# Performance work log

Measured on AMD Instinct MI355X. Metric: run time of the kernel, lower is better.

The kernel has to match this reference:

```python
import jax, jax.numpy as jnp
import numpy as np

B, S, E, H = 8, 1024, 512, 8
NEG = -1e10


def setup_inputs() -> dict:
    key = jax.random.key(0)
    ks = jax.random.split(key, 8)
    k = jax.random.normal(ks[0], (B, S, E), dtype=jnp.float32)
    v = jax.random.normal(ks[1], (B, S, E), dtype=jnp.float32)
    q = jax.random.normal(ks[2], (B, S, E), dtype=jnp.float32)
    # causal mask, broadcastable like torch masked_fill
    mask = jnp.tril(jnp.ones((S, S), dtype=jnp.int32))[None, None]
    sc = 1.0 / np.sqrt(E)
    Wk = jax.random.normal(ks[3], (H * E, E), dtype=jnp.float32) * sc
    Wq = jax.random.normal(ks[4], (H * E, E), dtype=jnp.float32) * sc
    Wv = jax.random.normal(ks[5], (H * E, E), dtype=jnp.float32) * sc
    Wo = jax.random.normal(ks[6], (E, H * E), dtype=jnp.float32) * (1.0 / np.sqrt(H * E))
    bo = jnp.zeros((E,), dtype=jnp.float32)
    return {"k": k, "v": v, "q": q, "mask": mask,
            "Wk": Wk, "Wq": Wq, "Wv": Wv, "Wo": Wo, "bo": bo}


def reference(k, v, q, mask, Wk, Wq, Wv, Wo, bo):
    b, q_len, e = q.shape
    k_len, v_len = k.shape[1], v.shape[1]
    h = Wk.shape[0] // e
    scale = jnp.sqrt(jnp.asarray(e // h, dtype=jnp.float32))
    # projections E -> H*E (torch Linear: x @ W.T)
    wk = (k @ Wk.T).reshape(b, h, k_len, e)   # raw reshape, matches torch .view
    wq = (q @ Wq.T).reshape(b, h, q_len, e)
    wv = (v @ Wv.T).reshape(b, h, v_len, e)
    energy = jnp.einsum('bhqe,bhke->bhqk', wq, wk)
    energy = jnp.where(mask == 0, NEG, energy)  # mask applied BEFORE scaling, as in source
    energy = energy / scale
    attn = jax.nn.softmax(energy, axis=-1)
    f = jnp.einsum('bhqk,bhke->bhqe', attn, wv)
    f = jnp.transpose(f, (0, 2, 1, 3)).reshape(b, q_len, h * e)
    return f @ Wo.T + bo
```

## Files before the change

### kernel.cpp

```cpp
#include <hip/hip_runtime.h>


typedef _Float16 half8 __attribute__((ext_vector_type(8)));
typedef _Float16 half4v __attribute__((ext_vector_type(4)));
typedef float f32x4 __attribute__((ext_vector_type(4)));

typedef __attribute__((address_space(3))) unsigned int lds_u32_t;
typedef __attribute__((address_space(1))) unsigned int g_u32_t;

__device__ __forceinline__ void glds16(const void* g, void* l) {
  __builtin_amdgcn_global_load_lds((const g_u32_t*)g, (lds_u32_t*)l, 16, 0, 0);
}

template <int NT>
__device__ __forceinline__ void gemm128x256_core(const _Float16* __restrict__ A,
                                                 const _Float16* __restrict__ B,
                                                 int lda, int ldb,
                                                 _Float16* smem, f32x4 (&acc)[4][8]) {
  int tid = (int)threadIdx.x;
  int w = tid >> 6, lane = tid & 63;
  int wr2 = (w >> 1) * 32;
  int wc2 = (w & 1) * 64;
  int lr = lane & 15, hi = lane >> 4;
  int sp = ((((lane & 1) << 2) + hi) ^ ((lr >> 1) & 7)) << 3;
  int aBase = (wr2 + (lr >> 1)) * 64 + sp;
  int bBase = 4096 + (wc2 + (lr >> 1)) * 64 + sp;

  int srcA[2], srcB[4], dstA[2], dstB[4];
#pragma unroll
  for (int e = 0; e < 2; e++) {
    int X = e * 4096 + tid * 16;
    int rp = X >> 7;
    int s = ((X >> 4) & 7) ^ (rp & 7);
    srcA[e] = (2 * rp + (s >> 2)) * lda + ((s & 3) << 3);
    dstA[e] = e * 2048 + w * 512;
  }
#pragma unroll
  for (int e = 0; e < 4; e++) {
    int X = e * 4096 + tid * 16;
    int rp = X >> 7;
    int s = ((X >> 4) & 7) ^ (rp & 7);
    srcB[e] = (2 * rp + (s >> 2)) * ldb + ((s & 3) << 3);
    dstB[e] = 4096 + e * 2048 + w * 512;
  }

#pragma unroll
  for (int e = 0; e < 2; e++) glds16(A + srcA[e], smem + dstA[e]);
#pragma unroll
  for (int e = 0; e < 4; e++) glds16(B + srcB[e], smem + dstB[e]);
  if (NT > 1) {
#pragma unroll
    for (int e = 0; e < 2; e++) glds16(A + srcA[e] + 32, smem + 12288 + dstA[e]);
#pragma unroll
    for (int e = 0; e < 4; e++) glds16(B + srcB[e] + 32, smem + 12288 + dstB[e]);
  }

#pragma unroll
  for (int t = 0; t < NT; t++) {
    if (t + 1 < NT) asm volatile("s_waitcnt vmcnt(6)" ::: "memory");
    else            asm volatile("s_waitcnt vmcnt(0)" ::: "memory");
    __builtin_amdgcn_s_barrier();
    __builtin_amdgcn_sched_barrier(0);
    const _Float16* As = smem + (t % 3) * 12288;
    half8 a[4], b[4], c[4];
#pragma unroll
    for (int ni = 0; ni < 4; ni++) b[ni] = *(const half8*)&As[bBase + ni * 512];
#pragma unroll
    for (int mi = 0; mi < 4; mi++) a[mi] = *(const half8*)&As[aBase + mi * 512];
    if (t + 2 < NT) {
      _Float16* nb = smem + ((t + 2) % 3) * 12288;
#pragma unroll
      for (int e = 0; e < 2; e++) glds16(A + srcA[e] + (t + 2) * 32, nb + dstA[e]);
#pragma unroll
      for (int e = 0; e < 4; e++) glds16(B + srcB[e] + (t + 2) * 32, nb + dstB[e]);
    }
    __builtin_amdgcn_sched_barrier(0);
#pragma unroll
    for (int ni = 0; ni < 4; ni++)
      c[ni] = *(const half8*)&As[bBase + (ni + 4) * 512];
    __builtin_amdgcn_s_setprio(1);
#pragma unroll
    for (int mi = 0; mi < 4; mi++)
#pragma unroll
      for (int ni = 0; ni < 4; ni++)
        acc[mi][ni] = __builtin_amdgcn_mfma_f32_16x16x32_f16(a[mi], b[ni],
                                                             acc[mi][ni], 0, 0, 0);
#pragma unroll
    for (int mi = 0; mi < 4; mi++)
#pragma unroll
      for (int ni = 0; ni < 4; ni++)
        acc[mi][ni + 4] = __builtin_amdgcn_mfma_f32_16x16x32_f16(a[mi], c[ni],
                                                                 acc[mi][ni + 4], 0, 0, 0);
    __builtin_amdgcn_s_setprio(0);
    asm volatile("s_waitcnt lgkmcnt(0)" ::: "memory");
    __builtin_amdgcn_sched_barrier(0);
  }
  __syncthreads();
}

__device__ __forceinline__ void epilogue128x256(f32x4 (&acc)[4][8], _Float16* lds,
                                                _Float16* Cp, size_t cOff,
                                                int i0, int j0, int ldc) {
  int tid = (int)threadIdx.x;
  int w = tid >> 6, lane = tid & 63;
  int wr = (w >> 1) * 64, wc = (w & 1) * 128;
  int r0 = (lane >> 4) * 4, cl = lane & 15;
  _Float16* T = lds + w * 4096;
#pragma unroll
  for (int h = 0; h < 2; h++) {
#pragma unroll
    for (int mi = 0; mi < 4; mi++)
#pragma unroll
      for (int ni = 0; ni < 4; ni++) {
        int colb = ni * 16 + cl;
#pragma unroll
        for (int r = 0; r < 4; r++) {
          int row = mi * 16 + r0 + r;
          T[row * 64 + ((((colb >> 3) ^ row) & 7) << 3) + (colb & 7)] =
              (_Float16)acc[mi][h * 4 + ni][r];
        }
      }
#pragma unroll
    for (int st = 0; st < 8; st++) {
      int row = st * 8 + (lane >> 3);
      int c8 = lane & 7;
      half8 hh = *(const half8*)&T[row * 64 + (((c8 ^ row) & 7) << 3)];
      *(half8*)(Cp + cOff + (size_t)(i0 + wr + row) * ldc + j0 + wc + h * 64 + c8 * 8) = hh;
    }
  }
}

template <int HG>
__global__ __launch_bounds__(256, 2) void proj256(const _Float16* __restrict__ in16,
                                                  const _Float16* __restrict__ W16,
                                                  _Float16* __restrict__ Qp,
                                                  _Float16* __restrict__ Kp,
                                                  _Float16* __restrict__ Vp) {
  __shared__ __align__(16) _Float16 smem[36864];
  int x = (int)blockIdx.x, Y = (int)blockIdx.y;
  int work = (x & 7) * (HG * 16) + (x >> 3);
  int it = work >> 4, jt = work & 15;
  const _Float16* A = in16 + (size_t)Y * HG * 524288 + (size_t)it * 65536;
  const _Float16* B = W16 + (size_t)Y * 2097152 + (size_t)jt * 131072;
  _Float16* C = (Y == 0 ? Qp : (Y == 1 ? Kp : Vp));
  f32x4 acc[4][8] = {};
  gemm128x256_core<16>(A, B, 512, 512, smem, acc);
  epilogue128x256(acc, smem, C, 0, it * 128, jt * 256, 4096);
}

template <int HG>
__global__ __launch_bounds__(256, 2) void vwo256(const _Float16* __restrict__ Vp,
                                                 const _Float16* __restrict__ WoG,
                                                 _Float16* __restrict__ VWo) {
  __shared__ __align__(16) _Float16 smem[36864];
  int x = (int)blockIdx.x, Y = (int)blockIdx.y, Z = (int)blockIdx.z;
  size_t z = (size_t)Z * HG + Y;
  int i0 = (x >> 2) * 128, j0 = (x & 3) * 256;
  const _Float16* A = WoG + (size_t)Y * 512 + (size_t)i0 * 4096;
  const _Float16* B = Vp + z * 524288 + (size_t)j0 * 512;
  f32x4 acc[4][8] = {};
  gemm128x256_core<16>(A, B, 4096, 512, smem, acc);
  epilogue128x256(acc, smem, VWo, z * 524288, i0, j0, 1024);
}

template <int HG>
__global__ __launch_bounds__(256, 2) void energy256(const _Float16* __restrict__ Qp,
                                                    const _Float16* __restrict__ Kp,
                                                    _Float16* __restrict__ E) {
  __shared__ __align__(16) _Float16 smem[36864];
  int x = (int)blockIdx.x, Y = (int)blockIdx.y, Z = (int)blockIdx.z;
  size_t z = (size_t)Z * HG + Y;
  int ti, tj;
  if (x < 8)       { tj = 0; ti = x; }
  else if (x < 14) { tj = 1; ti = x - 6; }
  else if (x < 18) { tj = 2; ti = x - 10; }
  else             { tj = 3; ti = x - 12; }
  int i0 = ti * 128, j0 = tj * 256;
  const _Float16* A = Qp + z * 524288 + (size_t)i0 * 512;
  const _Float16* B = Kp + z * 524288 + (size_t)j0 * 512;
  f32x4 acc[4][8] = {};
  gemm128x256_core<16>(A, B, 512, 512, smem, acc);
  epilogue128x256(acc, smem, E, z * 1048576, i0, j0, 1024);
}

template <int HL>
__device__ __forceinline__ void gemm_core(const _Float16* A, const _Float16* B,
                                          int lda, int ldb, int kmax,
                                          long sAh, long sBh,
                                          _Float16* As, _Float16* Bs,
                                          f32x4 (&acc)[4][4]) {
  int tid = (int)threadIdx.x;
  int w = tid >> 6, lane = tid & 63;
  int wr = (w >> 1) * 64, wc = (w & 1) * 64;
  int lr = lane & 15, lk = (lane >> 4) * 8;
  int srow = lane >> 2, sseg = (lane & 3) * 8;

  for (int h = 0; h < HL; h++) {
    const _Float16* Ah = A + (size_t)h * sAh;
    const _Float16* Bh = B + (size_t)h * sBh;
    for (int k0 = 0; k0 < kmax; k0 += 64) {
      __syncthreads();
#pragma unroll
      for (int p = 0; p < 2; p++)
#pragma unroll
        for (int t = 0; t < 2; t++) {
          glds16(Ah + (size_t)(w * 32 + t * 16 + srow) * lda + k0 + p * 32 + sseg,
                 As + p * 4096 + (w * 32 + t * 16) * 32);
          glds16(Bh + (size_t)(w * 32 + t * 16 + srow) * ldb + k0 + p * 32 + sseg,
                 Bs + p * 4096 + (w * 32 + t * 16) * 32);
        }
      __syncthreads();
#pragma unroll
      for (int p = 0; p < 2; p++) {
        half8 a[4], b[4];
#pragma unroll
        for (int mi = 0; mi < 4; mi++)
          a[mi] = *(half8*)&As[p * 4096 + (wr + mi * 16 + lr) * 32 + lk];
#pragma unroll
        for (int ni = 0; ni < 4; ni++)
          b[ni] = *(half8*)&Bs[p * 4096 + (wc + ni * 16 + lr) * 32 + lk];
#pragma unroll
        for (int mi = 0; mi < 4; mi++)
#pragma unroll
          for (int ni = 0; ni < 4; ni++)
            acc[mi][ni] =
                __builtin_amdgcn_mfma_f32_16x16x32_f16(a[mi], b[ni], acc[mi][ni], 0, 0, 0);
      }
    }
  }
}

__device__ __forceinline__ void epilogue_atomic(f32x4 (&acc)[4][4], float* Cp,
                                                size_t cOff, int i0, int j0, int ldc) {
  int tid = (int)threadIdx.x;
  int w = tid >> 6, lane = tid & 63;
  int wr = (w >> 1) * 64, wc = (w & 1) * 64;
  int r0 = (lane >> 4) * 4, col = lane & 15;
#pragma unroll
  for (int mi = 0; mi < 4; mi++)
#pragma unroll
    for (int ni = 0; ni < 4; ni++)
#pragma unroll
      for (int r = 0; r < 4; r++)
        unsafeAtomicAdd(Cp + cOff + (size_t)(i0 + wr + mi * 16 + r0 + r) * ldc +
                            j0 + wc + ni * 16 + col,
                        acc[mi][ni][r]);
}

template <int HG, int HL>
__global__ __launch_bounds__(256) void pv_kernel(const _Float16* __restrict__ E,
                                                 const _Float16* __restrict__ VWo,
                                                 float* __restrict__ out) {
  __shared__ __align__(16) _Float16 smem[17408];
  int x = (int)blockIdx.x, Y = (int)blockIdx.y, Z = (int)blockIdx.z;
  int i0 = (x >> 2) * 128, j0 = (x & 3) * 128;
  int kmax = i0 + 128;
  const _Float16* A = E + ((size_t)Z * HG + (size_t)Y * HL) * 1048576 + (size_t)i0 * 1024;
  const _Float16* B = VWo + ((size_t)Z * HG + (size_t)Y * HL) * 524288 + (size_t)j0 * 1024;
  f32x4 acc[4][4] = {};
  gemm_core<HL>(A, B, 1024, 1024, kmax, 1048576, 524288, smem, smem + 8192, acc);
  epilogue_atomic(acc, out, (size_t)Z * 524288, i0, j0, 512);
}

__global__ __launch_bounds__(256) void softmax_rows(void* __restrict__ Ep) {
  int R = (int)blockIdx.x * 4 + ((int)threadIdx.x >> 6);
  int lane = (int)threadIdx.x & 63;
  int i = R & 1023;
  int nt = (i >> 8) + 1;
  _Float16* row = (_Float16*)Ep + (size_t)R * 1024;
  float x[16];
  float m = -3.0e38f;
#pragma unroll
  for (int t = 0; t < 4; t++) {
    if (t < nt) {
      int j0 = t * 256 + lane * 4;
      half4v h = *(const half4v*)(row + j0);
#pragma unroll
      for (int c = 0; c < 4; c++) {
        float v = (j0 + c <= i) ? (float)h[c] * 0.125f : -3.0e38f;
        x[t * 4 + c] = v;
        m = fmaxf(m, v);
      }
    }
  }
#pragma unroll
  for (int s = 32; s > 0; s >>= 1) m = fmaxf(m, __shfl_xor(m, s, 64));
  float p[16];
  float sum = 0.0f;
#pragma unroll
  for (int t = 0; t < 4; t++) {
    if (t < nt) {
#pragma unroll
      for (int c = 0; c < 4; c++) {
        p[t * 4 + c] = exp2f((x[t * 4 + c] - m) * 1.44269504f);
        sum += p[t * 4 + c];
      }
    }
  }
#pragma unroll
  for (int s = 32; s > 0; s >>= 1) sum += __shfl_xor(sum, s, 64);
  float inv = 1.0f / sum;
#pragma unroll
  for (int t = 0; t < 4; t++) {
    if (t < nt) {
      int j0 = t * 256 + lane * 4;
      half4v h;
#pragma unroll
      for (int c = 0; c < 4; c++) h[c] = (_Float16)(p[t * 4 + c] * inv);
      *(half4v*)(row + j0) = h;
    }
  }
}

__global__ __launch_bounds__(256) void wbconv(const float* __restrict__ Wq,
                                              const float* __restrict__ Wk,
                                              const float* __restrict__ Wv,
                                              const float* __restrict__ Wo,
                                              _Float16* __restrict__ W16,
                                              float* __restrict__ out,
                                              const float* __restrict__ bo) {
  int bx = (int)blockIdx.x;
  if (bx < 4096) {
    size_t base = ((size_t)bx * 256 + threadIdx.x) * 8;
    int wid = (int)(base >> 21);
    size_t off = base & 2097151;
    const float* src = wid == 0 ? Wq : (wid == 1 ? Wk : (wid == 2 ? Wv : Wo));
    float4 a = *(const float4*)(src + off);
    float4 b = *(const float4*)(src + off + 4);
    half8 h;
    h[0] = (_Float16)a.x; h[1] = (_Float16)a.y; h[2] = (_Float16)a.z; h[3] = (_Float16)a.w;
    h[4] = (_Float16)b.x; h[5] = (_Float16)b.y; h[6] = (_Float16)b.z; h[7] = (_Float16)b.w;
    *(half8*)(W16 + base) = h;
  } else {
    size_t idx = ((size_t)(bx - 4096) * 256 + threadIdx.x) * 4;
    *(float4*)(out + idx) = *(const float4*)(bo + (idx & 511));
  }
}

template <int HG>
__global__ __launch_bounds__(256) void inconv(const float* __restrict__ q,
                                              const float* __restrict__ k,
                                              const float* __restrict__ v,
                                              _Float16* __restrict__ dst) {
  int Y = (int)blockIdx.y;
  size_t base = ((size_t)blockIdx.x * 256 + threadIdx.x) * 8;
  size_t b = base / (HG * 65536);
  size_t within = base - b * (HG * 65536);
  const float* src = (Y == 0 ? q : (Y == 1 ? k : v)) + b * 524288 + within;
  float4 a = ((const float4*)src)[0];
  float4 c = ((const float4*)src)[1];
  half8 h;
  h[0] = (_Float16)a.x; h[1] = (_Float16)a.y; h[2] = (_Float16)a.z; h[3] = (_Float16)a.w;
  h[4] = (_Float16)c.x; h[5] = (_Float16)c.y; h[6] = (_Float16)c.z; h[7] = (_Float16)c.w;
  *(half8*)(dst + (size_t)Y * HG * 524288 + base) = h;
}

template <int HG>
static void run_pipeline(const float* q_in, const float* k_in, const float* v_in,
                         const float* Wq, const float* Wk, const float* Wv,
                         const float* Wo, const float* bo, float* out, char* ws,
                         hipStream_t stream) {
  const int NG = 8 / HG;
  const long zc = 8 * HG;
  _Float16* W16 = (_Float16*)ws;
  _Float16* in16 = W16 + 8388608;
  _Float16* Qp = in16 + 3L * HG * 524288;
  _Float16* Kp = Qp + zc * 524288;
  _Float16* VWo = Kp + zc * 524288;
  _Float16* E = VWo + zc * 524288;
  _Float16* Vp = E;
  _Float16* Wo16 = W16 + 3 * 2097152;
  dim3 blk(256);

  wbconv<<<dim3(8192), blk, 0, stream>>>(Wq, Wk, Wv, Wo, W16, out, bo);

  constexpr int HL = (HG >= 2) ? 2 : 1;
  constexpr int YS = HG / HL;

  for (int g = 0; g < NG; g++) {
    inconv<HG><<<dim3(HG * 256, 3), blk, 0, stream>>>(
        q_in + (size_t)g * HG * 65536, k_in + (size_t)g * HG * 65536,
        v_in + (size_t)g * HG * 65536, in16);

    proj256<HG><<<dim3(HG * 128, 3), blk, 0, stream>>>(in16, W16, Qp, Kp, Vp);

    vwo256<HG><<<dim3(16, HG, 8), blk, 0, stream>>>(
        Vp, Wo16 + (size_t)g * HG * 512, VWo);

    energy256<HG><<<dim3(20, HG, 8), blk, 0, stream>>>(Qp, Kp, E);

    softmax_rows<<<dim3(zc * 256), blk, 0, stream>>>(E);

    pv_kernel<HG, HL><<<dim3(32, YS, 8), blk, 0, stream>>>(E, VWo, out);
  }
}

extern "C" void kernel_launch(void* const* d_in, const int* in_sizes, int n_in,
                              void* d_out, int out_size, void* d_ws, size_t ws_size,
                              hipStream_t stream) {
  const float* k_in = (const float*)d_in[0];
  const float* v_in = (const float*)d_in[1];
  const float* q_in = (const float*)d_in[2];
  const float* Wk = (const float*)d_in[4];
  const float* Wq = (const float*)d_in[5];
  const float* Wv = (const float*)d_in[6];
  const float* Wo = (const float*)d_in[7];
  const float* bo = (const float*)d_in[8];
  float* out = (float*)d_out;
  char* ws = (char*)d_ws;

  if (ws_size >= (size_t)197132288)
    run_pipeline<4>(q_in, k_in, v_in, Wq, Wk, Wv, Wo, bo, out, ws, stream);
  else if (ws_size >= (size_t)106954752)
    run_pipeline<2>(q_in, k_in, v_in, Wq, Wk, Wv, Wo, bo, out, ws, stream);
  else
    run_pipeline<1>(q_in, k_in, v_in, Wq, Wk, Wv, Wo, bo, out, ws, stream);
}
```

Baseline: 529.8 us.

## Rewrite PV GEMM with triple-buffered async LDS pipeline and swizzled layout

Replaces the synchronous PV GEMM core with a kernel that keeps two K-tiles in flight through a three-slot LDS ring filled by global_load_lds. It waits with explicit vmcnt counts and issues the next loads while the MFMAs run, instead of using two __syncthreads per 64-wide step. It also switches to an XOR-swizzled shared-memory layout, which should cut LDS bank conflicts. Other additions are launch_bounds occupancy 2 and s_setprio around the MFMA block. The hand-managed waitcnt and barrier ordering adds a risk of subtle races if a count is wrong.

Result: no change. 539.2 us (+1.8%).

```diff
diff --git a/kernel.cpp b/kernel.cpp
--- a/kernel.cpp
+++ b/kernel.cpp
@@ -183,53 +183,6 @@
   epilogue128x256(acc, smem, E, z * 1048576, i0, j0, 1024);
 }
 
-template <int HL>
-__device__ __forceinline__ void gemm_core(const _Float16* A, const _Float16* B,
-                                          int lda, int ldb, int kmax,
-                                          long sAh, long sBh,
-                                          _Float16* As, _Float16* Bs,
-                                          f32x4 (&acc)[4][4]) {
-  int tid = (int)threadIdx.x;
-  int w = tid >> 6, lane = tid & 63;
-  int wr = (w >> 1) * 64, wc = (w & 1) * 64;
-  int lr = lane & 15, lk = (lane >> 4) * 8;
-  int srow = lane >> 2, sseg = (lane & 3) * 8;
-
-  for (int h = 0; h < HL; h++) {
-    const _Float16* Ah = A + (size_t)h * sAh;
-    const _Float16* Bh = B + (size_t)h * sBh;
-    for (int k0 = 0; k0 < kmax; k0 += 64) {
-      __syncthreads();
-#pragma unroll
-      for (int p = 0; p < 2; p++)
-#pragma unroll
-        for (int t = 0; t < 2; t++) {
-          glds16(Ah + (size_t)(w * 32 + t * 16 + srow) * lda + k0 + p * 32 + sseg,
-                 As + p * 4096 + (w * 32 + t * 16) * 32);
-          glds16(Bh + (size_t)(w * 32 + t * 16 + srow) * ldb + k0 + p * 32 + sseg,
-                 Bs + p * 4096 + (w * 32 + t * 16) * 32);
-        }
-      __syncthreads();
-#pragma unroll
-      for (int p = 0; p < 2; p++) {
-        half8 a[4], b[4];
-#pragma unroll
-        for (int mi = 0; mi < 4; mi++)
-          a[mi] = *(half8*)&As[p * 4096 + (wr + mi * 16 + lr) * 32 + lk];
-#pragma unroll
-        for (int ni = 0; ni < 4; ni++)
-          b[ni] = *(half8*)&Bs[p * 4096 + (wc + ni * 16 + lr) * 32 + lk];
-#pragma unroll
-        for (int mi = 0; mi < 4; mi++)
-#pragma unroll
-          for (int ni = 0; ni < 4; ni++)
-            acc[mi][ni] =
-                __builtin_amdgcn_mfma_f32_16x16x32_f16(a[mi], b[ni], acc[mi][ni], 0, 0, 0);
-      }
-    }
-  }
-}
-
 __device__ __forceinline__ void epilogue_atomic(f32x4 (&acc)[4][4], float* Cp,
                                                 size_t cOff, int i0, int j0, int ldc) {
   int tid = (int)threadIdx.x;
@@ -248,17 +201,86 @@
 }
 
 template <int HG, int HL>
-__global__ __launch_bounds__(256) void pv_kernel(const _Float16* __restrict__ E,
-                                                 const _Float16* __restrict__ VWo,
-                                                 float* __restrict__ out) {
-  __shared__ __align__(16) _Float16 smem[17408];
+__global__ __launch_bounds__(256, 2) void pv2(const _Float16* __restrict__ E,
+                                              const _Float16* __restrict__ VWo,
+                                              float* __restrict__ out) {
+  __shared__ __align__(16) _Float16 smem[24576];
   int x = (int)blockIdx.x, Y = (int)blockIdx.y, Z = (int)blockIdx.z;
   int i0 = (x >> 2) * 128, j0 = (x & 3) * 128;
-  int kmax = i0 + 128;
-  const _Float16* A = E + ((size_t)Z * HG + (size_t)Y * HL) * 1048576 + (size_t)i0 * 1024;
-  const _Float16* B = VWo + ((size_t)Z * HG + (size_t)Y * HL) * 524288 + (size_t)j0 * 1024;
+  size_t z0 = (size_t)Z * HG + (size_t)Y * HL;
+  const _Float16* EA = E + z0 * 1048576 + (size_t)i0 * 1024;
+  const _Float16* BB = VWo + z0 * 524288 + (size_t)j0 * 1024;
+
+  int tid = (int)threadIdx.x;
+  int w = tid >> 6, lane = tid & 63;
+  int wr2 = (w >> 1) * 32;
+  int wc2 = (w & 1) * 32;
+  int lr = lane & 15, hi = lane >> 4;
+  int sp = ((((lane & 1) << 2) + hi) ^ ((lr >> 1) & 7)) << 3;
+  int aBase = (wr2 + (lr >> 1)) * 64 + sp;
+  int bBase = 4096 + (wc2 + (lr >> 1)) * 64 + sp;
+
+  int srcP[2], dstE_[2];
+#pragma unroll
+  for (int e = 0; e < 2; e++) {
+    int X = e * 4096 + tid * 16;
+    int rp = X >> 7;
+    int s = ((X >> 4) & 7) ^ (rp & 7);
+    srcP[e] = (2 * rp + (s >> 2)) * 1024 + ((s & 3) << 3);
+    dstE_[e] = e * 2048 + w * 512;
+  }
+
+  int NTr = (i0 >> 5) + 4;
+  int total = HL * NTr;
+
+#pragma unroll
+  for (int e = 0; e < 2; e++) glds16(EA + srcP[e], smem + dstE_[e]);
+#pragma unroll
+  for (int e = 0; e < 2; e++) glds16(BB + srcP[e], smem + 4096 + dstE_[e]);
+#pragma unroll
+  for (int e = 0; e < 2; e++) glds16(EA + srcP[e] + 32, smem + 8192 + dstE_[e]);
+#pragma unroll
+  for (int e = 0; e < 2; e++) glds16(BB + srcP[e] + 32, smem + 12288 + dstE_[e]);
+
   f32x4 acc[4][4] = {};
-  gemm_core<HL>(A, B, 1024, 1024, kmax, 1048576, 524288, smem, smem + 8192, acc);
+  int hs = 0, ts = 2;
+  int bufc = 0, bufs = 2;
+  for (int s = 0; s < total; s++) {
+    if (s + 1 < total) asm volatile("s_waitcnt vmcnt(4)" ::: "memory");
+    else               asm volatile("s_waitcnt vmcnt(0)" ::: "memory");
+    __builtin_amdgcn_s_barrier();
+    __builtin_amdgcn_sched_barrier(0);
+    const _Float16* As = smem + bufc * 8192;
+    half8 a[4], b[4];
+#pragma unroll
+    for (int ni = 0; ni < 4; ni++) b[ni] = *(const half8*)&As[bBase + ni * 512];
+#pragma unroll
+    for (int mi = 0; mi < 4; mi++) a[mi] = *(const half8*)&As[aBase + mi * 512];
+    if (s + 2 < total) {
+      const _Float16* Ah = EA + (size_t)hs * 1048576;
+      const _Float16* Bh = BB + (size_t)hs * 524288;
+      _Float16* nb = smem + bufs * 8192;
+      int ko = ts * 32;
+#pragma unroll
+      for (int e = 0; e < 2; e++) glds16(Ah + srcP[e] + ko, nb + dstE_[e]);
+#pragma unroll
+      for (int e = 0; e < 2; e++) glds16(Bh + srcP[e] + ko, nb + 4096 + dstE_[e]);
+      ts++; if (ts == NTr) { ts = 0; hs++; }
+      bufs = (bufs == 2) ? 0 : bufs + 1;
+    }
+    __builtin_amdgcn_sched_barrier(0);
+    __builtin_amdgcn_s_setprio(1);
+#pragma unroll
+    for (int mi = 0; mi < 4; mi++)
+#pragma unroll
+      for (int ni = 0; ni < 4; ni++)
+        acc[mi][ni] = __builtin_amdgcn_mfma_f32_16x16x32_f16(a[mi], b[ni],
+                                                             acc[mi][ni], 0, 0, 0);
+    __builtin_amdgcn_s_setprio(0);
+    asm volatile("s_waitcnt lgkmcnt(0)" ::: "memory");
+    __builtin_amdgcn_sched_barrier(0);
+    bufc = (bufc == 2) ? 0 : bufc + 1;
+  }
   epilogue_atomic(acc, out, (size_t)Z * 524288, i0, j0, 512);
 }
 
@@ -391,7 +413,7 @@
 
     softmax_rows<<<dim3(zc * 256), blk, 0, stream>>>(E);
 
-    pv_kernel<HG, HL><<<dim3(32, YS, 8), blk, 0, stream>>>(E, VWo, out);
+    pv2<HG, HL><<<dim3(32, YS, 8), blk, 0, stream>>>(E, VWo, out);
   }
 }
 
```
